# Optimization experiments

Hardware: AMD Instinct MI355X
Metric: run time of the kernel (lower is better)

The kernel has to match this reference:

```python
import jax, jax.numpy as jnp
import numpy as np

D_MODEL = 1024
NUM_HEADS = 16
HEAD_DIM = D_MODEL // NUM_HEADS


def setup_inputs() -> dict:
    key = jax.random.key(0)
    ks = jax.random.split(key, 5)
    s = 1.0 / np.sqrt(D_MODEL)
    return {
        "x": jax.random.normal(ks[0], (2, 2048, D_MODEL), dtype=jnp.float32),
        "Wqkv": jax.random.normal(ks[1], (3 * D_MODEL, D_MODEL), dtype=jnp.float32) * s,
        "bqkv": jax.random.normal(ks[2], (3 * D_MODEL,), dtype=jnp.float32) * s,
        "Wo": jax.random.normal(ks[3], (D_MODEL, D_MODEL), dtype=jnp.float32) * s,
        "bo": jax.random.normal(ks[4], (D_MODEL,), dtype=jnp.float32) * s,
    }


def reference(x, Wqkv, bqkv, Wo, bo):
    B, S, D = x.shape
    H, hd = NUM_HEADS, HEAD_DIM
    # fused QKV projection (torch Linear: x @ W.T + b)
    qkv = x @ Wqkv.T + bqkv                      # [B, S, 3D]
    qkv = qkv.reshape(B, S, H, 3 * hd).transpose(0, 2, 1, 3)  # [B, H, S, 3hd]
    q, k, v = jnp.split(qkv, 3, axis=-1)         # each [B, H, S, hd]
    scaled = jnp.einsum("bhqd,bhkd->bhqk", q, k) / jnp.sqrt(jnp.float32(hd))
    # module applies causal mask when its `mask` flag is False (the default)
    causal = jnp.tril(jnp.ones((S, S), dtype=bool))
    scaled = jnp.where(causal, scaled, -jnp.inf)
    attn = jax.nn.softmax(scaled, axis=-1)       # [B, H, S, S]
    values = jnp.einsum("bhqk,bhkd->bhqd", attn, v)  # [B, H, S, hd]
    # NOTE: original uses .reshape (not transpose-then-reshape) on the
    # [B, H, S, hd] tensor directly — reproduce that exact layout.
    values = values.reshape(B, S, H * hd)
    out = values @ Wo.T + bo                     # [B, S, D]
    return out
```

## Files before the change

kernel.cpp:

```cpp
#include <hip/hip_runtime.h>

typedef __attribute__((ext_vector_type(8))) short bf16x8;
typedef __attribute__((ext_vector_type(4))) float f32x4;

#define D_MODEL 1024
#define NHEADS 16
#define HDIM 64
#define SEQ 2048
#define BATCH 2
#define MROWS (BATCH*SEQ)
#define NQKV (3*D_MODEL)
#define QSCALE 0.1803368801111204f
#define PEXP_OFF 12.0f
#define CSTR 144

__device__ __forceinline__ unsigned short f2bf(float f) {
  unsigned int u = __float_as_uint(f);
  u += 0x7FFF + ((u >> 16) & 1);
  return (unsigned short)(u >> 16);
}
__device__ __forceinline__ unsigned int pack2bf(float a, float b) {
#if __has_builtin(__builtin_amdgcn_cvt_pk_bf16_f32)
  auto r = __builtin_amdgcn_cvt_pk_bf16_f32(a, b);
  unsigned int u; __builtin_memcpy(&u, &r, 4);
  return u;
#else
  return ((unsigned int)f2bf(b) << 16) | (unsigned int)f2bf(a);
#endif
}

__device__ __forceinline__ void gload16(const void* g, void* l) {
  __builtin_amdgcn_global_load_lds((const __attribute__((address_space(1))) void*)g,
                                   (__attribute__((address_space(3))) void*)l, 16, 0, 0);
}

#define N4_X     1048576
#define N4_WQKV   786432
#define N4_WO     262144
__global__ void cvt_all_kernel(const float4* __restrict__ x,
                               const float4* __restrict__ wqkv,
                               const float4* __restrict__ wo,
                               ushort4* __restrict__ xb,
                               ushort4* __restrict__ wqkvb,
                               ushort4* __restrict__ wob) {
  int i = blockIdx.x * blockDim.x + threadIdx.x;
  const float4* s; ushort4* d; int j;
  if (i < N4_X)                { s = x;    d = xb;    j = i; }
  else if (i < N4_X + N4_WQKV) { s = wqkv; d = wqkvb; j = i - N4_X; }
  else                         { s = wo;   d = wob;   j = i - (N4_X + N4_WQKV); }
  float4 v = s[j];
  ushort4 o;
  o.x = f2bf(v.x); o.y = f2bf(v.y); o.z = f2bf(v.z); o.w = f2bf(v.w);
  d[j] = o;
}

template<int MODE, int BM>
__global__ __launch_bounds__(256) void gemm_bt_kernel(
    const unsigned short* __restrict__ A,
    const unsigned short* __restrict__ Bm,
    const float* __restrict__ bias,
    float* __restrict__ outF,
    unsigned short* __restrict__ Qb,
    unsigned short* __restrict__ Kb,
    unsigned short* __restrict__ VTb,
    int M, int N, int K)
{
  constexpr int MI = BM / 32;
  constexpr int STG = BM*32 + 128*32;
  constexpr int SHSZ = (MODE == 0 && 128*CSTR > 2*STG) ? 128*CSTR : 2*STG;
  __shared__ __align__(16) unsigned short Sh[SHSZ];
  const int tid = threadIdx.x;
  const int wave = tid >> 6, lane = tid & 63;
  const int lm = lane & 15, quad = lane >> 4;
  const int wm = (wave >> 1) * (BM/2), wn = (wave & 1) * 64;
  const int m0 = blockIdx.y * BM, n0 = blockIdx.x * 128;

  f32x4 acc[MI][4] = {};

  auto stage_in = [&](int k0, int sb) {
    unsigned short* As = Sh + sb*STG;
    unsigned short* Bs = As + BM*32;
#pragma unroll
    for (int i = 0; i < BM/64; i++) {
      int ch = i*256 + tid;
      int r = ch >> 2, cg = (ch & 3) ^ ((r >> 1) & 3);
      gload16(&A[(size_t)(m0 + r) * K + k0 + cg*8], &As[ch*8]);
    }
#pragma unroll
    for (int i = 0; i < 2; i++) {
      int ch = i*256 + tid;
      int r = ch >> 2, cg = (ch & 3) ^ ((r >> 1) & 3);
      gload16(&Bm[(size_t)(n0 + r) * K + k0 + cg*8], &Bs[ch*8]);
    }
  };

  stage_in(0, 0);
  for (int k0 = 0; k0 < K; k0 += 32) {
    const int cur = (k0 >> 5) & 1;
    __syncthreads();
    if (k0 + 32 < K) stage_in(k0 + 32, cur ^ 1);
    const unsigned short* As = Sh + cur*STG;
    const unsigned short* Bs = As + BM*32;
    bf16x8 af[MI], bfr[4];
#pragma unroll
    for (int mi = 0; mi < MI; mi++) {
      int r = wm + mi*16 + lm;
      af[mi] = *(const bf16x8*)&As[(r*4 + (quad ^ ((r >> 1) & 3))) * 8];
    }
#pragma unroll
    for (int ni = 0; ni < 4; ni++) {
      int r = wn + ni*16 + lm;
      bfr[ni] = *(const bf16x8*)&Bs[(r*4 + (quad ^ ((r >> 1) & 3))) * 8];
    }
#pragma unroll
    for (int mi = 0; mi < MI; mi++)
#pragma unroll
      for (int ni = 0; ni < 4; ni++)
        acc[mi][ni] = __builtin_amdgcn_mfma_f32_16x16x32_bf16(af[mi], bfr[ni], acc[mi][ni], 0, 0, 0);
  }

  if (MODE == 1) {
#pragma unroll
    for (int mi = 0; mi < MI; mi++)
#pragma unroll
      for (int ni = 0; ni < 4; ni++)
#pragma unroll
        for (int r = 0; r < 4; r++) {
          int row = m0 + wm + mi*16 + quad*4 + r;
          int col = n0 + wn + ni*16 + lm;
          outF[(size_t)row * N + col] = acc[mi][ni][r] + bias[col];
        }
  } else {
    __syncthreads();
#pragma unroll
    for (int mi = 0; mi < MI; mi++)
#pragma unroll
      for (int ni = 0; ni < 4; ni++)
#pragma unroll
        for (int r = 0; r < 4; r++) {
          int row_l = wm + mi*16 + quad*4 + r;
          int col_l = wn + ni*16 + lm;
          int col = n0 + col_l;
          float v = acc[mi][ni][r] + bias[col];
          if (((col % 192) >> 6) == 0) v *= QSCALE;
          Sh[row_l*CSTR + col_l] = f2bf(v);
        }
    __syncthreads();
#pragma unroll
    for (int i = 0; i < 8; i++) {
      int lin = i*256 + tid;
      int row_l = lin >> 4, cc = (lin & 15) * 8;
      int col = n0 + cc;
      int h = col / 192, rr = col - h*192;
      int ty = rr >> 6, e = rr & 63;
      if (ty < 2) {
        uint4 d = *(const uint4*)&Sh[row_l*CSTR + cc];
        int row = m0 + row_l;
        int b = row >> 11, s = row & (SEQ - 1);
        unsigned short* dst = ty ? Kb : Qb;
        *(uint4*)&dst[((size_t)(b*NHEADS + h)*SEQ + s)*HDIM + e] = d;
      }
    }
#pragma unroll
    for (int i = 0; i < 8; i++) {
      int lin = i*256 + tid;
      int col_l = lin & 127, s8 = (lin >> 7) * 8;
      int col = n0 + col_l;
      int h = col / 192, rr = col - h*192;
      if ((rr >> 6) == 2) {
        int e = rr & 63;
        unsigned short tmp[8];
#pragma unroll
        for (int j = 0; j < 8; j++) tmp[j] = Sh[(s8 + j)*CSTR + col_l];
        int row = m0 + s8;
        int b = row >> 11, s = row & (SEQ - 1);
        size_t vb = ((size_t)(b*NHEADS + h)*HDIM + e)*SEQ;
        int pos = (s & ~31) | (((s >> 2) & 3) << 3) | (((s >> 4) & 1) << 2);
        *(uint2*)&VTb[vb + pos]     = *(const uint2*)&tmp[0];
        *(uint2*)&VTb[vb + pos + 8] = *(const uint2*)&tmp[4];
      }
    }
  }
}

__global__ __launch_bounds__(1024, 4) void flash_attn_kernel(
    const unsigned short* __restrict__ Qb,
    const unsigned short* __restrict__ Kb,
    const unsigned short* __restrict__ VTb,
    unsigned short* __restrict__ Ob)
{
  const int tid = threadIdx.x;
  const int wave = tid >> 6, lane = tid & 63;
  const int lm = lane & 15, quad = lane >> 4;
  const int qg = wave >> 1;
  const int kh = wave & 1;
  const int bx = blockIdx.x;
  const int bh = (bx & 7) * 4 + (bx >> 3);
  const int pr = blockIdx.y;
  const int t0 = 15 - pr, t1 = pr;
  const int nk0 = t0 + 1;
  const int ntot = nk0 + t1 + 1;

  __shared__ __align__(16) unsigned short Sh[2][128*64 + 64*128];
  __shared__ __align__(16) float Scr[8*64*17];

  const unsigned short* Qbh  = Qb  + (size_t)bh*SEQ*HDIM;
  const unsigned short* Kbh  = Kb  + (size_t)bh*SEQ*HDIM;
  const unsigned short* VTbh = VTb + (size_t)bh*HDIM*SEQ;

  auto stage_in = [&](int k0, int sb) {
    {
      int ch = tid;
      int r = ch >> 3, cg = (ch & 7) ^ (r & 7);
      gload16(&Kbh[(size_t)(k0 + r)*HDIM + cg*8], &Sh[sb][ch*8]);
    }
    {
      int ch = tid;
      int e = ch >> 4, cg = (ch & 15) ^ (e & 7);
      gload16(&VTbh[(size_t)e*SEQ + k0 + cg*8], &Sh[sb][128*64 + ch*8]);
    }
  };

  int rowq = t0*128 + qg*16;
  int query = rowq + lm;
  bf16x8 qf[2];
#pragma unroll
  for (int kc = 0; kc < 2; kc++)
    qf[kc] = *(const bf16x8*)&Qbh[(size_t)query*HDIM + kc*32 + quad*8];

  union { unsigned short us[8]; bf16x8 v; } ones_u;
#pragma unroll
  for (int j = 0; j < 8; j++) ones_u.us[j] = 0x3F80;
  const bf16x8 onesv = ones_u.v;

  f32x4 o[4] = {};
  f32x4 lacc = {};

  stage_in(0, 0);
  for (int s = 0; s < ntot; s++) {
    const int kt = (s < nk0) ? s : s - nk0;
    const int k0 = kt * 128;
    const int cur = s & 1;
    __syncthreads();
    if (s + 1 < ntot) {
      int sn = s + 1;
      int ktn = (sn < nk0) ? sn : sn - nk0;
      stage_in(ktn * 128, cur ^ 1);
    }
    const unsigned short* Ksc = &Sh[cur][0];
    const unsigned short* Vsc = &Sh[cur][128*64];

    f32x4 sc[4] = {};
    __builtin_amdgcn_s_setprio(1);
#pragma unroll
    for (int kc = 0; kc < 2; kc++)
#pragma unroll
      for (int mi = 0; mi < 4; mi++) {
        int r = (kh*4 + mi)*16 + lm, cc = kc*4 + quad;
        bf16x8 kf = *(const bf16x8*)&Ksc[(r*8 + (cc ^ (r & 7))) * 8];
        sc[mi] = __builtin_amdgcn_mfma_f32_16x16x32_bf16(kf, qf[kc], sc[mi], 0, 0, 0);
      }
    __builtin_amdgcn_s_setprio(0);

    if (k0 + kh*64 + 63 > rowq) {
#pragma unroll
      for (int mi = 0; mi < 4; mi++)
#pragma unroll
        for (int r = 0; r < 4; r++) {
          int key = k0 + (kh*4 + mi)*16 + quad*4 + r;
          if (key > query) sc[mi][r] = -1e30f;
        }
    }

    float p[4][4];
#pragma unroll
    for (int mi = 0; mi < 4; mi++)
#pragma unroll
      for (int r2 = 0; r2 < 4; r2++)
        p[mi][r2] = exp2f(sc[mi][r2] - PEXP_OFF);

    __builtin_amdgcn_s_setprio(1);
#pragma unroll
    for (int c = 0; c < 2; c++) {
      union { unsigned int w[4]; bf16x8 v; } pu;
      pu.w[0] = pack2bf(p[2*c][0],   p[2*c][1]);
      pu.w[1] = pack2bf(p[2*c][2],   p[2*c][3]);
      pu.w[2] = pack2bf(p[2*c+1][0], p[2*c+1][1]);
      pu.w[3] = pack2bf(p[2*c+1][2], p[2*c+1][3]);
      lacc = __builtin_amdgcn_mfma_f32_16x16x32_bf16(onesv, pu.v, lacc, 0, 0, 0);
#pragma unroll
      for (int ei = 0; ei < 4; ei++) {
        int e = ei*16 + lm, cc = (2*kh + c)*4 + quad;
        bf16x8 vf = *(const bf16x8*)&Vsc[(e*16 + (cc ^ (e & 7))) * 8];
        o[ei] = __builtin_amdgcn_mfma_f32_16x16x32_bf16(vf, pu.v, o[ei], 0, 0, 0);
      }
    }
    __builtin_amdgcn_s_setprio(0);

    if (s == nk0 - 1 || s == ntot - 1) {
      float* mine = Scr + (qg*64 + lane)*17;
      if (kh) {
        mine[16] = lacc[0];
#pragma unroll
        for (int ei = 0; ei < 4; ei++)
#pragma unroll
          for (int r2 = 0; r2 < 4; r2++) mine[ei*4 + r2] = o[ei][r2];
      }
      __syncthreads();
      if (!kh) {
        float inv = 1.0f / (lacc[0] + mine[16]);
        size_t obase = ((size_t)bh*SEQ + query) * HDIM;
#pragma unroll
        for (int ei = 0; ei < 4; ei++) {
          float v0 = (o[ei][0] + mine[ei*4 + 0]) * inv;
          float v1 = (o[ei][1] + mine[ei*4 + 1]) * inv;
          float v2 = (o[ei][2] + mine[ei*4 + 2]) * inv;
          float v3 = (o[ei][3] + mine[ei*4 + 3]) * inv;
          uint2 u;
          u.x = pack2bf(v0, v1);
          u.y = pack2bf(v2, v3);
          *(uint2*)&Ob[obase + ei*16 + quad*4] = u;
        }
      }
      if (s == nk0 - 1) {
        rowq = t1*128 + qg*16;
        query = rowq + lm;
#pragma unroll
        for (int kc = 0; kc < 2; kc++)
          qf[kc] = *(const bf16x8*)&Qbh[(size_t)query*HDIM + kc*32 + quad*8];
#pragma unroll
        for (int ei = 0; ei < 4; ei++)
#pragma unroll
          for (int r2 = 0; r2 < 4; r2++) o[ei][r2] = 0.f;
#pragma unroll
      for (int r2 = 0; r2 < 4; r2++) lacc[r2] = 0.f;
      }
    }
  }
}

extern "C" void kernel_launch(void* const* d_in, const int* in_sizes, int n_in,
                              void* d_out, int out_size, void* d_ws, size_t ws_size,
                              hipStream_t stream) {
  const float* x    = (const float*)d_in[0];
  const float* Wqkv = (const float*)d_in[1];
  const float* bqkv = (const float*)d_in[2];
  const float* Wo   = (const float*)d_in[3];
  const float* bo   = (const float*)d_in[4];
  float* out = (float*)d_out;

  char* ws = (char*)d_ws;
  unsigned short* Xbf    = (unsigned short*)(ws);
  unsigned short* Wqkvbf = (unsigned short*)(ws + 8388608);
  unsigned short* Wobf   = (unsigned short*)(ws + 14680064);
  unsigned short* Qb     = (unsigned short*)(ws + 16777216);
  unsigned short* Kb     = (unsigned short*)(ws + 25165824);
  unsigned short* VTb    = (unsigned short*)(ws + 33554432);
  unsigned short* Ob     = (unsigned short*)(ws + 41943040);

  cvt_all_kernel<<<8192, 256, 0, stream>>>(
      (const float4*)x, (const float4*)Wqkv, (const float4*)Wo,
      (ushort4*)Xbf, (ushort4*)Wqkvbf, (ushort4*)Wobf);

  gemm_bt_kernel<0,128><<<dim3(24, 32), 256, 0, stream>>>(
      Xbf, Wqkvbf, bqkv, nullptr, Qb, Kb, VTb, MROWS, NQKV, D_MODEL);

  flash_attn_kernel<<<dim3(32, 8), 1024, 0, stream>>>(Qb, Kb, VTb, Ob);

  gemm_bt_kernel<1,64><<<dim3(8, 64), 256, 0, stream>>>(
      Ob, Wobf, bo, out, nullptr, nullptr, nullptr, MROWS, D_MODEL, D_MODEL);
}
```

Measured before the change: 179.9 us.

## Remap flash-attention waves to 32 queries by 32 keys to reuse K/V fragments

Changes the wave decomposition in the flash attention kernel from 8 query groups × 2 key halves to 4 query groups × 4 key quarters. Each wave now handles two 16-row query tiles, so every K and V fragment read from LDS feeds two MFMAs. This halves LDS fragment reads per MFMA. The cost is more accumulator registers per wave and a four-way cross-wave reduction through shared memory, with an extra barrier at finalisation.

```diff
diff --git a/kernel.cpp b/kernel.cpp
--- a/kernel.cpp
+++ b/kernel.cpp
@@ -192,8 +192,8 @@
   const int tid = threadIdx.x;
   const int wave = tid >> 6, lane = tid & 63;
   const int lm = lane & 15, quad = lane >> 4;
-  const int qg = wave >> 1;
-  const int kh = wave & 1;
+  const int qg = wave >> 2;
+  const int kh = wave & 3;
   const int bx = blockIdx.x;
   const int bh = (bx & 7) * 4 + (bx >> 3);
   const int pr = blockIdx.y;
@@ -202,7 +202,7 @@
   const int ntot = nk0 + t1 + 1;
 
   __shared__ __align__(16) unsigned short Sh[2][128*64 + 64*128];
-  __shared__ __align__(16) float Scr[8*64*17];
+  __shared__ __align__(16) float Scr[4*3*64*20];
 
   const unsigned short* Qbh  = Qb  + (size_t)bh*SEQ*HDIM;
   const unsigned short* Kbh  = Kb  + (size_t)bh*SEQ*HDIM;
@@ -221,20 +221,24 @@
     }
   };
 
-  int rowq = t0*128 + qg*16;
-  int query = rowq + lm;
-  bf16x8 qf[2];
-#pragma unroll
-  for (int kc = 0; kc < 2; kc++)
-    qf[kc] = *(const bf16x8*)&Qbh[(size_t)query*HDIM + kc*32 + quad*8];
+  int rowq = t0*128 + qg*32;
+  int query[2];
+  bf16x8 qf[2][2];
+#pragma unroll
+  for (int g = 0; g < 2; g++) {
+    query[g] = rowq + g*16 + lm;
+#pragma unroll
+    for (int kc = 0; kc < 2; kc++)
+      qf[g][kc] = *(const bf16x8*)&Qbh[(size_t)query[g]*HDIM + kc*32 + quad*8];
+  }
 
   union { unsigned short us[8]; bf16x8 v; } ones_u;
 #pragma unroll
   for (int j = 0; j < 8; j++) ones_u.us[j] = 0x3F80;
   const bf16x8 onesv = ones_u.v;
 
-  f32x4 o[4] = {};
-  f32x4 lacc = {};
+  f32x4 o[2][4] = {};
+  f32x4 lacc[2] = {};
 
   stage_in(0, 0);
   for (int s = 0; s < ntot; s++) {
@@ -250,90 +254,110 @@
     const unsigned short* Ksc = &Sh[cur][0];
     const unsigned short* Vsc = &Sh[cur][128*64];
 
-    f32x4 sc[4] = {};
+    f32x4 sc[2][2] = {};
     __builtin_amdgcn_s_setprio(1);
 #pragma unroll
     for (int kc = 0; kc < 2; kc++)
 #pragma unroll
-      for (int mi = 0; mi < 4; mi++) {
-        int r = (kh*4 + mi)*16 + lm, cc = kc*4 + quad;
+      for (int mi = 0; mi < 2; mi++) {
+        int r = (kh*2 + mi)*16 + lm, cc = kc*4 + quad;
         bf16x8 kf = *(const bf16x8*)&Ksc[(r*8 + (cc ^ (r & 7))) * 8];
-        sc[mi] = __builtin_amdgcn_mfma_f32_16x16x32_bf16(kf, qf[kc], sc[mi], 0, 0, 0);
+        sc[0][mi] = __builtin_amdgcn_mfma_f32_16x16x32_bf16(kf, qf[0][kc], sc[0][mi], 0, 0, 0);
+        sc[1][mi] = __builtin_amdgcn_mfma_f32_16x16x32_bf16(kf, qf[1][kc], sc[1][mi], 0, 0, 0);
       }
     __builtin_amdgcn_s_setprio(0);
 
-    if (k0 + kh*64 + 63 > rowq) {
-#pragma unroll
-      for (int mi = 0; mi < 4; mi++)
-#pragma unroll
-        for (int r = 0; r < 4; r++) {
-          int key = k0 + (kh*4 + mi)*16 + quad*4 + r;
-          if (key > query) sc[mi][r] = -1e30f;
-        }
-    }
-
-    float p[4][4];
-#pragma unroll
-    for (int mi = 0; mi < 4; mi++)
-#pragma unroll
-      for (int r2 = 0; r2 < 4; r2++)
-        p[mi][r2] = exp2f(sc[mi][r2] - PEXP_OFF);
-
+    if (k0 + kh*32 + 31 > rowq) {
+#pragma unroll
+      for (int g = 0; g < 2; g++)
+#pragma unroll
+        for (int mi = 0; mi < 2; mi++)
+#pragma unroll
+          for (int r = 0; r < 4; r++) {
+            int key = k0 + (kh*2 + mi)*16 + quad*4 + r;
+            if (key > query[g]) sc[g][mi][r] = -1e30f;
+          }
+    }
+
+    float p[2][2][4];
+#pragma unroll
+    for (int g = 0; g < 2; g++)
+#pragma unroll
+      for (int mi = 0; mi < 2; mi++)
+#pragma unroll
+        for (int r2 = 0; r2 < 4; r2++)
+          p[g][mi][r2] = exp2f(sc[g][mi][r2] - PEXP_OFF);
+
+    bf16x8 pf[2];
     __builtin_amdgcn_s_setprio(1);
 #pragma unroll
-    for (int c = 0; c < 2; c++) {
+    for (int g = 0; g < 2; g++) {
       union { unsigned int w[4]; bf16x8 v; } pu;
-      pu.w[0] = pack2bf(p[2*c][0],   p[2*c][1]);
-      pu.w[1] = pack2bf(p[2*c][2],   p[2*c][3]);
-      pu.w[2] = pack2bf(p[2*c+1][0], p[2*c+1][1]);
-      pu.w[3] = pack2bf(p[2*c+1][2], p[2*c+1][3]);
-      lacc = __builtin_amdgcn_mfma_f32_16x16x32_bf16(onesv, pu.v, lacc, 0, 0, 0);
-#pragma unroll
-      for (int ei = 0; ei < 4; ei++) {
-        int e = ei*16 + lm, cc = (2*kh + c)*4 + quad;
-        bf16x8 vf = *(const bf16x8*)&Vsc[(e*16 + (cc ^ (e & 7))) * 8];
-        o[ei] = __builtin_amdgcn_mfma_f32_16x16x32_bf16(vf, pu.v, o[ei], 0, 0, 0);
-      }
+      pu.w[0] = pack2bf(p[g][0][0], p[g][0][1]);
+      pu.w[1] = pack2bf(p[g][0][2], p[g][0][3]);
+      pu.w[2] = pack2bf(p[g][1][0], p[g][1][1]);
+      pu.w[3] = pack2bf(p[g][1][2], p[g][1][3]);
+      pf[g] = pu.v;
+      lacc[g] = __builtin_amdgcn_mfma_f32_16x16x32_bf16(onesv, pu.v, lacc[g], 0, 0, 0);
+    }
+#pragma unroll
+    for (int ei = 0; ei < 4; ei++) {
+      int e = ei*16 + lm, cc = kh*4 + quad;
+      bf16x8 vf = *(const bf16x8*)&Vsc[(e*16 + (cc ^ (e & 7))) * 8];
+      o[0][ei] = __builtin_amdgcn_mfma_f32_16x16x32_bf16(vf, pf[0], o[0][ei], 0, 0, 0);
+      o[1][ei] = __builtin_amdgcn_mfma_f32_16x16x32_bf16(vf, pf[1], o[1][ei], 0, 0, 0);
     }
     __builtin_amdgcn_s_setprio(0);
 
     if (s == nk0 - 1 || s == ntot - 1) {
-      float* mine = Scr + (qg*64 + lane)*17;
-      if (kh) {
-        mine[16] = lacc[0];
-#pragma unroll
-        for (int ei = 0; ei < 4; ei++)
-#pragma unroll
-          for (int r2 = 0; r2 < 4; r2++) mine[ei*4 + r2] = o[ei][r2];
-      }
-      __syncthreads();
-      if (!kh) {
-        float inv = 1.0f / (lacc[0] + mine[16]);
-        size_t obase = ((size_t)bh*SEQ + query) * HDIM;
-#pragma unroll
-        for (int ei = 0; ei < 4; ei++) {
-          float v0 = (o[ei][0] + mine[ei*4 + 0]) * inv;
-          float v1 = (o[ei][1] + mine[ei*4 + 1]) * inv;
-          float v2 = (o[ei][2] + mine[ei*4 + 2]) * inv;
-          float v3 = (o[ei][3] + mine[ei*4 + 3]) * inv;
-          uint2 u;
-          u.x = pack2bf(v0, v1);
-          u.y = pack2bf(v2, v3);
-          *(uint2*)&Ob[obase + ei*16 + quad*4] = u;
-        }
+#pragma unroll
+      for (int g = 0; g < 2; g++) {
+        if (kh) {
+          float* slot = Scr + ((qg*3 + (kh - 1))*64 + lane)*20;
+#pragma unroll
+          for (int ei = 0; ei < 4; ei++) *(f32x4*)&slot[ei*4] = o[g][ei];
+          slot[16] = lacc[g][0];
+        }
+        __syncthreads();
+        if (!kh) {
+          float lt = lacc[g][0];
+          f32x4 ot[4];
+#pragma unroll
+          for (int ei = 0; ei < 4; ei++) ot[ei] = o[g][ei];
+#pragma unroll
+          for (int w = 0; w < 3; w++) {
+            const float* rs = Scr + ((qg*3 + w)*64 + lane)*20;
+            lt += rs[16];
+#pragma unroll
+            for (int ei = 0; ei < 4; ei++) ot[ei] += *(const f32x4*)&rs[ei*4];
+          }
+          float inv = 1.0f / lt;
+          size_t obase = ((size_t)bh*SEQ + query[g]) * HDIM;
+#pragma unroll
+          for (int ei = 0; ei < 4; ei++) {
+            uint2 u;
+            u.x = pack2bf(ot[ei][0]*inv, ot[ei][1]*inv);
+            u.y = pack2bf(ot[ei][2]*inv, ot[ei][3]*inv);
+            *(uint2*)&Ob[obase + ei*16 + quad*4] = u;
+          }
+        }
+        __syncthreads();
       }
       if (s == nk0 - 1) {
-        rowq = t1*128 + qg*16;
-        query = rowq + lm;
-#pragma unroll
-        for (int kc = 0; kc < 2; kc++)
-          qf[kc] = *(const bf16x8*)&Qbh[(size_t)query*HDIM + kc*32 + quad*8];
-#pragma unroll
-        for (int ei = 0; ei < 4; ei++)
-#pragma unroll
-          for (int r2 = 0; r2 < 4; r2++) o[ei][r2] = 0.f;
-#pragma unroll
-      for (int r2 = 0; r2 < 4; r2++) lacc[r2] = 0.f;
+        rowq = t1*128 + qg*32;
+#pragma unroll
+        for (int g = 0; g < 2; g++) {
+          query[g] = rowq + g*16 + lm;
+#pragma unroll
+          for (int kc = 0; kc < 2; kc++)
+            qf[g][kc] = *(const bf16x8*)&Qbh[(size_t)query[g]*HDIM + kc*32 + quad*8];
+#pragma unroll
+          for (int ei = 0; ei < 4; ei++)
+#pragma unroll
+            for (int r2 = 0; r2 < 4; r2++) o[g][ei][r2] = 0.f;
+#pragma unroll
+          for (int r2 = 0; r2 < 4; r2++) lacc[g][r2] = 0.f;
+        }
       }
     }
   }
```

Result: slower. 183.8 us (+2.1%).
